# Kernel tuning notes

Measured on AMD Instinct MI355X. Metric: run time of the kernel, lower is better.

## Reference

```python
import jax, jax.numpy as jnp
import numpy as np

# Config constants (BayesianTripletConfig defaults)
MARGIN = 0.3
UNCERTAINTY_WEIGHT = 0.05
MIN_U = 1e-6
MAX_U = 1.0
TEMPERATURE = 1.0
EPS = 1e-8
B, D, N_CLASSES = 512, 256, 64


def setup_inputs() -> dict:
    key = jax.random.key(0)
    k1, k2, k3 = jax.random.split(key, 3)
    embeddings = jax.random.normal(k1, (B, D), dtype=jnp.float32)
    uncertainties = jax.random.uniform(k2, (B, D), dtype=jnp.float32)
    labels = jax.random.randint(k3, (B,), 0, N_CLASSES)
    return {"embeddings": embeddings, "uncertainties": uncertainties, "labels": labels}


def _loss(embeddings, uncertainties, labels):
    u = jnp.clip(uncertainties, MIN_U, MAX_U)
    u = jnp.where(jnp.isnan(u) | jnp.isinf(u), MIN_U, u)

    # ---- uncertainty-aware euclidean distances (vectorized) ----
    diff = embeddings[:, None, :] - embeddings[None, :, :]        # [B,B,D]
    dist = jnp.sqrt(jnp.sum(diff * diff, axis=-1)) + EPS           # [B,B]
    # d(dist_ij)/d(e_i,d) = diff_ijd / dist_ij ; propagate anchor-side uncertainty u_i
    partial = diff / dist[:, :, None]                              # [B,B,D]
    dist_unc = jnp.sqrt(jnp.sum(partial * partial * (u[:, None, :] ** 2), axis=-1) + EPS)  # [B,B]

    # ---- hardest triplet mining (vectorized over anchors) ----
    same = labels[:, None] == labels[None, :]
    eye = jnp.eye(labels.shape[0], dtype=bool)
    pos_mask = same & ~eye
    neg_mask = ~same
    neg_inf = jnp.float32(-1e30)
    pos_inf = jnp.float32(1e30)
    hardest_pos = jnp.argmax(jnp.where(pos_mask, dist, neg_inf), axis=1)  # farthest positive
    hardest_neg = jnp.argmin(jnp.where(neg_mask, dist, pos_inf), axis=1)  # closest negative
    valid = pos_mask.any(axis=1) & neg_mask.any(axis=1)

    rows = jnp.arange(labels.shape[0])
    d_pos = dist[rows, hardest_pos]
    d_neg = dist[rows, hardest_neg]
    u_pos = dist_unc[rows, hardest_pos]
    u_neg = dist_unc[rows, hardest_neg]

    # ---- probabilistic (gaussian) uncertainty-aware margin loss per triplet ----
    sigma = jnp.sqrt(u_pos ** 2 + u_neg ** 2 + EPS)
    margin_eff = MARGIN + UNCERTAINTY_WEIGHT * sigma               # adaptive_margin=True
    z = (d_pos - d_neg + margin_eff) / (sigma * TEMPERATURE)
    per_triplet = sigma * TEMPERATURE * jax.nn.softplus(z)         # smooth uncertainty-weighted hinge

    n_valid = jnp.maximum(jnp.sum(valid.astype(jnp.float32)), 1.0)
    main_loss = jnp.sum(jnp.where(valid, per_triplet, 0.0)) / n_valid

    # ---- uncertainty regularization (uncertainty_regularization=True) ----
    unc_reg = jnp.mean(u)
    total = main_loss + UNCERTAINTY_WEIGHT * unc_reg
    total = jnp.where(jnp.isnan(total) | jnp.isinf(total), 0.0, total)
    return total


def reference(embeddings, uncertainties, labels):
    return _loss(embeddings, uncertainties, labels)
```

## Files before the change

kernel.cpp:

```cpp
#include <hip/hip_runtime.h>
#include <math.h>

#define B 512
#define D 256
#define MARGIN 0.3f
#define UW 0.05f
#define MIN_U 1e-6f
#define EPS 1e-8f

#define TI 16
#define TJ 64
#define BK 64
#define NJT (B / TJ)

typedef unsigned long long ull;


static __device__ inline ull shfl_xor_u64(ull v, int m) {
    unsigned int lo = (unsigned int)v;
    unsigned int hi = (unsigned int)(v >> 32);
    lo = __shfl_xor(lo, m, 64);
    hi = __shfl_xor(hi, m, 64);
    return ((ull)hi << 32) | lo;
}

static __device__ inline ull bcast_u64_lane0(ull v) {
    unsigned int lo = (unsigned int)v;
    unsigned int hi = (unsigned int)(v >> 32);
    lo = (unsigned int)__shfl((int)lo, 0, 64);
    hi = (unsigned int)__shfl((int)hi, 0, 64);
    return ((ull)hi << 32) | lo;
}

__global__ __launch_bounds__(256) void dist_mine(const float* __restrict__ emb,
                                                 const int* __restrict__ labels,
                                                 ull* __restrict__ pmax_part,
                                                 ull* __restrict__ nmin_part,
                                                 unsigned int* __restrict__ counter) {
    const int jt = blockIdx.x;
    const int it = blockIdx.y;
    const int t  = threadIdx.x;
    const int row  = t >> 4;
    const int col4 = (t & 15) * 4;

    if (jt == 0 && it == 0 && t == 0) *counter = 0u;

    __shared__ float As[BK][TI + 1];
    __shared__ float Bs[BK][TJ + 4];
    __shared__ int labI[TI], labJ[TJ];

    const int gi0 = it * TI;
    const int gj0 = jt * TJ;
    if (t < TI) labI[t] = labels[gi0 + t];
    if (t < TJ) labJ[t] = labels[gj0 + t];

    float a0 = 0.f, a1 = 0.f, a2 = 0.f, a3 = 0.f;

    for (int kc = 0; kc < D; kc += BK) {
        __syncthreads();
        {
            const int r = t >> 4;
            const int f = t & 15;
            float4 v = *reinterpret_cast<const float4*>(&emb[(size_t)(gi0 + r) * D + kc + f * 4]);
            As[f * 4 + 0][r] = v.x;
            As[f * 4 + 1][r] = v.y;
            As[f * 4 + 2][r] = v.z;
            As[f * 4 + 3][r] = v.w;
        }
#pragma unroll
        for (int g = 0; g < 4; ++g) {
            const int r = g * 16 + (t >> 4);
            const int f = t & 15;
            float4 v = *reinterpret_cast<const float4*>(&emb[(size_t)(gj0 + r) * D + kc + f * 4]);
            Bs[f * 4 + 0][r] = v.x;
            Bs[f * 4 + 1][r] = v.y;
            Bs[f * 4 + 2][r] = v.z;
            Bs[f * 4 + 3][r] = v.w;
        }
        __syncthreads();
#pragma unroll 8
        for (int k = 0; k < BK; ++k) {
            float a = As[k][row];
            float4 b = *reinterpret_cast<const float4*>(&Bs[k][col4]);
            float d;
            d = a - b.x; a0 = fmaf(d, d, a0);
            d = a - b.y; a1 = fmaf(d, d, a1);
            d = a - b.z; a2 = fmaf(d, d, a2);
            d = a - b.w; a3 = fmaf(d, d, a3);
        }
    }

    const int gi = gi0 + row;
    const int li = labI[row];
    ull pbest = 0ull;
    ull nbest = ~0ull;
    float accs[4] = {a0, a1, a2, a3};
#pragma unroll
    for (int c = 0; c < 4; ++c) {
        const int jj = col4 + c;
        const int gj = gj0 + jj;
        const float dist = sqrtf(accs[c]) + EPS;
        const int lj = labJ[jj];
        const ull fb = (ull)__float_as_uint(dist) << 32;
        if (li == lj && gi != gj) {
            ull e = fb | (unsigned int)(0xFFFFFFFFu - (unsigned int)gj);
            pbest = pbest > e ? pbest : e;
        }
        if (li != lj) {
            ull e = fb | (unsigned int)gj;
            nbest = nbest < e ? nbest : e;
        }
    }
#pragma unroll
    for (int m = 1; m < 16; m <<= 1) {
        ull p2 = shfl_xor_u64(pbest, m);
        ull n2 = shfl_xor_u64(nbest, m);
        pbest = pbest > p2 ? pbest : p2;
        nbest = nbest < n2 ? nbest : n2;
    }
    if ((t & 15) == 0) {
        pmax_part[(size_t)jt * B + gi] = pbest;
        nmin_part[(size_t)jt * B + gi] = nbest;
    }
}

__global__ __launch_bounds__(256) void finalize(const float* __restrict__ emb,
                                                const float* __restrict__ unc,
                                                const ull* __restrict__ pmax_part,
                                                const ull* __restrict__ nmin_part,
                                                float* __restrict__ blk_part,
                                                unsigned int* __restrict__ counter,
                                                float* __restrict__ out) {
    const int t = threadIdx.x;
    const int wave = t >> 6;
    const int lane = t & 63;
    __shared__ float red[4][3];
    __shared__ int s_last;

    float loss_sum = 0.f, nval = 0.f, usum = 0.f;
    const float4* emb4 = reinterpret_cast<const float4*>(emb);
    const float4* unc4 = reinterpret_cast<const float4*>(unc);

#pragma unroll
    for (int a = 0; a < 2; ++a) {
        const int i = blockIdx.x * 8 + wave * 2 + a;

        ull pe = 0ull, ne = ~0ull;
        if (lane < NJT) {
            pe = pmax_part[(size_t)lane * B + i];
            ne = nmin_part[(size_t)lane * B + i];
        }
#pragma unroll
        for (int m = 1; m < NJT; m <<= 1) {
            ull p2 = shfl_xor_u64(pe, m);
            ull n2 = shfl_xor_u64(ne, m);
            pe = pe > p2 ? pe : p2;
            ne = ne < n2 ? ne : n2;
        }
        pe = bcast_u64_lane0(pe);
        ne = bcast_u64_lane0(ne);

        const bool valid = (pe != 0ull) && (ne != ~0ull);
        const int jp = valid ? (int)(0xFFFFFFFFu - (unsigned int)pe) : i;
        const int jn = valid ? (int)(unsigned int)ne : i;
        const float dp = __uint_as_float((unsigned int)(pe >> 32));
        const float dn = __uint_as_float((unsigned int)(ne >> 32));

        float4 e = emb4[(size_t)i * 64 + lane];
        float4 u = unc4[(size_t)i * 64 + lane];
        float4 p = emb4[(size_t)jp * 64 + lane];
        float4 n = emb4[(size_t)jn * 64 + lane];
        float ux = fminf(fmaxf(u.x, MIN_U), 1.0f);
        float uy = fminf(fmaxf(u.y, MIN_U), 1.0f);
        float uz = fminf(fmaxf(u.z, MIN_U), 1.0f);
        float uw_ = fminf(fmaxf(u.w, MIN_U), 1.0f);

        float s0, s1, s2, d;
        d = e.x - p.x; s0 = ux * ux * d * d;
        d = e.y - p.y; s0 = fmaf(uy * uy, d * d, s0);
        d = e.z - p.z; s0 = fmaf(uz * uz, d * d, s0);
        d = e.w - p.w; s0 = fmaf(uw_ * uw_, d * d, s0);
        d = e.x - n.x; s1 = ux * ux * d * d;
        d = e.y - n.y; s1 = fmaf(uy * uy, d * d, s1);
        d = e.z - n.z; s1 = fmaf(uz * uz, d * d, s1);
        d = e.w - n.w; s1 = fmaf(uw_ * uw_, d * d, s1);
        s2 = ux + uy + uz + uw_;

#pragma unroll
        for (int m = 1; m < 64; m <<= 1) {
            s0 += __shfl_xor(s0, m, 64);
            s1 += __shfl_xor(s1, m, 64);
            s2 += __shfl_xor(s2, m, 64);
        }

        if (lane == 0) {
            usum += s2;
            if (valid) {
                const float up2 = s0 / (dp * dp) + EPS;
                const float un2 = s1 / (dn * dn) + EPS;
                const float sigma = sqrtf(up2 + un2 + EPS);
                const float z = (dp - dn + MARGIN + UW * sigma) / sigma;
                const float sp = fmaxf(z, 0.f) + log1pf(expf(-fabsf(z)));
                loss_sum += sigma * sp;
                nval += 1.0f;
            }
        }
    }

    if (lane == 0) {
        red[wave][0] = loss_sum;
        red[wave][1] = nval;
        red[wave][2] = usum;
    }
    __syncthreads();
    if (t == 0) {
        float l = red[0][0] + red[1][0] + red[2][0] + red[3][0];
        float v = red[0][1] + red[1][1] + red[2][1] + red[3][1];
        float s = red[0][2] + red[1][2] + red[2][2] + red[3][2];
        __hip_atomic_store(&blk_part[blockIdx.x * 3 + 0], l, __ATOMIC_RELAXED, __HIP_MEMORY_SCOPE_AGENT);
        __hip_atomic_store(&blk_part[blockIdx.x * 3 + 1], v, __ATOMIC_RELAXED, __HIP_MEMORY_SCOPE_AGENT);
        __hip_atomic_store(&blk_part[blockIdx.x * 3 + 2], s, __ATOMIC_RELAXED, __HIP_MEMORY_SCOPE_AGENT);
        unsigned int done = __hip_atomic_fetch_add(counter, 1u, __ATOMIC_ACQ_REL, __HIP_MEMORY_SCOPE_AGENT);
        s_last = (done == 63u);
    }
    __syncthreads();

    if (s_last && wave == 0) {
        float l = __hip_atomic_load(&blk_part[lane * 3 + 0], __ATOMIC_RELAXED, __HIP_MEMORY_SCOPE_AGENT);
        float v = __hip_atomic_load(&blk_part[lane * 3 + 1], __ATOMIC_RELAXED, __HIP_MEMORY_SCOPE_AGENT);
        float s = __hip_atomic_load(&blk_part[lane * 3 + 2], __ATOMIC_RELAXED, __HIP_MEMORY_SCOPE_AGENT);
#pragma unroll
        for (int m = 1; m < 64; m <<= 1) {
            l += __shfl_xor(l, m, 64);
            v += __shfl_xor(v, m, 64);
            s += __shfl_xor(s, m, 64);
        }
        if (lane == 0) {
            float total = l / fmaxf(v, 1.0f) + UW * (s / (float)(B * D));
            if (!isfinite(total)) total = 0.f;
            out[0] = total;
        }
    }
}

extern "C" void kernel_launch(void* const* d_in, const int* in_sizes, int n_in,
                              void* d_out, int out_size, void* d_ws, size_t ws_size,
                              hipStream_t stream) {
    const float* emb = (const float*)d_in[0];
    const float* unc = (const float*)d_in[1];
    const int* labels = (const int*)d_in[2];
    float* out = (float*)d_out;

    char* ws = (char*)d_ws;
    ull* pmax_part = (ull*)(ws);
    ull* nmin_part = (ull*)(ws + 32768);
    float* blk_part = (float*)(ws + 65536);
    unsigned int* counter = (unsigned int*)(ws + 66304);

    dim3 grid(NJT, B / TI);
    dist_mine<<<grid, 256, 0, stream>>>(emb, labels, pmax_part, nmin_part, counter);
    finalize<<<64, 256, 0, stream>>>(emb, unc, pmax_part, nmin_part, blk_part, counter, out);
}
```

Measured before the change: 72.60 us.

## Fuse distance mining and finalize into one cooperative kernel with grid syncs

Merges the two kernels into a single cooperative launch of 256 blocks. A grid-wide sync separates the mining phase from the per-anchor loss phase, and a second grid sync replaces the last-block atomic counter for the final reduction. The aim is to remove the second kernel launch and its inter-kernel gap. In exchange it pays for two grid barriers, and only half the waves do work in the finalize phase. Block 0 now reduces 256 partials across four waves.

```diff
diff --git a/kernel.cpp b/kernel.cpp
--- a/kernel.cpp
+++ b/kernel.cpp
@@ -1,4 +1,5 @@
 #include <hip/hip_runtime.h>
+#include <hip/hip_cooperative_groups.h>
 #include <math.h>
 
 #define B 512
@@ -14,6 +15,7 @@
 #define NJT (B / TJ)
 
 typedef unsigned long long ull;
+namespace cg = cooperative_groups;
 
 
 static __device__ inline ull shfl_xor_u64(ull v, int m) {
@@ -32,22 +34,25 @@
     return ((ull)hi << 32) | lo;
 }
 
-__global__ __launch_bounds__(256) void dist_mine(const float* __restrict__ emb,
-                                                 const int* __restrict__ labels,
-                                                 ull* __restrict__ pmax_part,
-                                                 ull* __restrict__ nmin_part,
-                                                 unsigned int* __restrict__ counter) {
-    const int jt = blockIdx.x;
-    const int it = blockIdx.y;
+__global__ __launch_bounds__(256) void fused(const float* __restrict__ emb,
+                                             const float* __restrict__ unc,
+                                             const int* __restrict__ labels,
+                                             ull* __restrict__ pmax_part,
+                                             ull* __restrict__ nmin_part,
+                                             float* __restrict__ blk_part,
+                                             float* __restrict__ out) {
+    const int bid = blockIdx.x;
+    const int jt = bid & (NJT - 1);
+    const int it = bid >> 3;
     const int t  = threadIdx.x;
     const int row  = t >> 4;
     const int col4 = (t & 15) * 4;
 
-    if (jt == 0 && it == 0 && t == 0) *counter = 0u;
-
     __shared__ float As[BK][TI + 1];
     __shared__ float Bs[BK][TJ + 4];
     __shared__ int labI[TI], labJ[TJ];
+    __shared__ float red[2][3];
+    __shared__ float fred[4][3];
 
     const int gi0 = it * TI;
     const int gj0 = jt * TJ;
@@ -90,65 +95,54 @@
         }
     }
 
-    const int gi = gi0 + row;
-    const int li = labI[row];
-    ull pbest = 0ull;
-    ull nbest = ~0ull;
-    float accs[4] = {a0, a1, a2, a3};
-#pragma unroll
-    for (int c = 0; c < 4; ++c) {
-        const int jj = col4 + c;
-        const int gj = gj0 + jj;
-        const float dist = sqrtf(accs[c]) + EPS;
-        const int lj = labJ[jj];
-        const ull fb = (ull)__float_as_uint(dist) << 32;
-        if (li == lj && gi != gj) {
-            ull e = fb | (unsigned int)(0xFFFFFFFFu - (unsigned int)gj);
-            pbest = pbest > e ? pbest : e;
-        }
-        if (li != lj) {
-            ull e = fb | (unsigned int)gj;
-            nbest = nbest < e ? nbest : e;
-        }
-    }
-#pragma unroll
-    for (int m = 1; m < 16; m <<= 1) {
-        ull p2 = shfl_xor_u64(pbest, m);
-        ull n2 = shfl_xor_u64(nbest, m);
-        pbest = pbest > p2 ? pbest : p2;
-        nbest = nbest < n2 ? nbest : n2;
-    }
-    if ((t & 15) == 0) {
-        pmax_part[(size_t)jt * B + gi] = pbest;
-        nmin_part[(size_t)jt * B + gi] = nbest;
-    }
-}
-
-__global__ __launch_bounds__(256) void finalize(const float* __restrict__ emb,
-                                                const float* __restrict__ unc,
-                                                const ull* __restrict__ pmax_part,
-                                                const ull* __restrict__ nmin_part,
-                                                float* __restrict__ blk_part,
-                                                unsigned int* __restrict__ counter,
-                                                float* __restrict__ out) {
-    const int t = threadIdx.x;
+    {
+        const int gi = gi0 + row;
+        const int li = labI[row];
+        ull pbest = 0ull;
+        ull nbest = ~0ull;
+        float accs[4] = {a0, a1, a2, a3};
+#pragma unroll
+        for (int c = 0; c < 4; ++c) {
+            const int jj = col4 + c;
+            const int gj = gj0 + jj;
+            const float dist = sqrtf(accs[c]) + EPS;
+            const int lj = labJ[jj];
+            const ull fb = (ull)__float_as_uint(dist) << 32;
+            if (li == lj && gi != gj) {
+                ull e = fb | (unsigned int)(0xFFFFFFFFu - (unsigned int)gj);
+                pbest = pbest > e ? pbest : e;
+            }
+            if (li != lj) {
+                ull e = fb | (unsigned int)gj;
+                nbest = nbest < e ? nbest : e;
+            }
+        }
+#pragma unroll
+        for (int m = 1; m < 16; m <<= 1) {
+            ull p2 = shfl_xor_u64(pbest, m);
+            ull n2 = shfl_xor_u64(nbest, m);
+            pbest = pbest > p2 ? pbest : p2;
+            nbest = nbest < n2 ? nbest : n2;
+        }
+        if ((t & 15) == 0) {
+            __hip_atomic_store(&pmax_part[(size_t)jt * B + gi], pbest, __ATOMIC_RELAXED, __HIP_MEMORY_SCOPE_AGENT);
+            __hip_atomic_store(&nmin_part[(size_t)jt * B + gi], nbest, __ATOMIC_RELAXED, __HIP_MEMORY_SCOPE_AGENT);
+        }
+    }
+
+    cg::this_grid().sync();
+
     const int wave = t >> 6;
     const int lane = t & 63;
-    __shared__ float red[4][3];
-    __shared__ int s_last;
-
-    float loss_sum = 0.f, nval = 0.f, usum = 0.f;
-    const float4* emb4 = reinterpret_cast<const float4*>(emb);
-    const float4* unc4 = reinterpret_cast<const float4*>(unc);
-
-#pragma unroll
-    for (int a = 0; a < 2; ++a) {
-        const int i = blockIdx.x * 8 + wave * 2 + a;
+
+    if (wave < 2) {
+        const int i = bid * 2 + wave;
+        float loss_sum = 0.f, nval = 0.f, usum = 0.f;
 
         ull pe = 0ull, ne = ~0ull;
         if (lane < NJT) {
-            pe = pmax_part[(size_t)lane * B + i];
-            ne = nmin_part[(size_t)lane * B + i];
+            pe = __hip_atomic_load(&pmax_part[(size_t)lane * B + i], __ATOMIC_RELAXED, __HIP_MEMORY_SCOPE_AGENT);
+            ne = __hip_atomic_load(&nmin_part[(size_t)lane * B + i], __ATOMIC_RELAXED, __HIP_MEMORY_SCOPE_AGENT);
         }
 #pragma unroll
         for (int m = 1; m < NJT; m <<= 1) {
@@ -166,6 +160,8 @@
         const float dp = __uint_as_float((unsigned int)(pe >> 32));
         const float dn = __uint_as_float((unsigned int)(ne >> 32));
 
+        const float4* emb4 = reinterpret_cast<const float4*>(emb);
+        const float4* unc4 = reinterpret_cast<const float4*>(unc);
         float4 e = emb4[(size_t)i * 64 + lane];
         float4 u = unc4[(size_t)i * 64 + lane];
         float4 p = emb4[(size_t)jp * 64 + lane];
@@ -194,41 +190,34 @@
         }
 
         if (lane == 0) {
-            usum += s2;
+            usum = s2;
             if (valid) {
                 const float up2 = s0 / (dp * dp) + EPS;
                 const float un2 = s1 / (dn * dn) + EPS;
                 const float sigma = sqrtf(up2 + un2 + EPS);
                 const float z = (dp - dn + MARGIN + UW * sigma) / sigma;
                 const float sp = fmaxf(z, 0.f) + log1pf(expf(-fabsf(z)));
-                loss_sum += sigma * sp;
-                nval += 1.0f;
+                loss_sum = sigma * sp;
+                nval = 1.0f;
             }
-        }
-    }
-
-    if (lane == 0) {
-        red[wave][0] = loss_sum;
-        red[wave][1] = nval;
-        red[wave][2] = usum;
+            red[wave][0] = loss_sum;
+            red[wave][1] = nval;
+            red[wave][2] = usum;
+        }
     }
     __syncthreads();
     if (t == 0) {
-        float l = red[0][0] + red[1][0] + red[2][0] + red[3][0];
-        float v = red[0][1] + red[1][1] + red[2][1] + red[3][1];
-        float s = red[0][2] + red[1][2] + red[2][2] + red[3][2];
-        __hip_atomic_store(&blk_part[blockIdx.x * 3 + 0], l, __ATOMIC_RELAXED, __HIP_MEMORY_SCOPE_AGENT);
-        __hip_atomic_store(&blk_part[blockIdx.x * 3 + 1], v, __ATOMIC_RELAXED, __HIP_MEMORY_SCOPE_AGENT);
-        __hip_atomic_store(&blk_part[blockIdx.x * 3 + 2], s, __ATOMIC_RELAXED, __HIP_MEMORY_SCOPE_AGENT);
-        unsigned int done = __hip_atomic_fetch_add(counter, 1u, __ATOMIC_ACQ_REL, __HIP_MEMORY_SCOPE_AGENT);
-        s_last = (done == 63u);
-    }
-    __syncthreads();
-
-    if (s_last && wave == 0) {
-        float l = __hip_atomic_load(&blk_part[lane * 3 + 0], __ATOMIC_RELAXED, __HIP_MEMORY_SCOPE_AGENT);
-        float v = __hip_atomic_load(&blk_part[lane * 3 + 1], __ATOMIC_RELAXED, __HIP_MEMORY_SCOPE_AGENT);
-        float s = __hip_atomic_load(&blk_part[lane * 3 + 2], __ATOMIC_RELAXED, __HIP_MEMORY_SCOPE_AGENT);
+        __hip_atomic_store(&blk_part[bid * 3 + 0], red[0][0] + red[1][0], __ATOMIC_RELAXED, __HIP_MEMORY_SCOPE_AGENT);
+        __hip_atomic_store(&blk_part[bid * 3 + 1], red[0][1] + red[1][1], __ATOMIC_RELAXED, __HIP_MEMORY_SCOPE_AGENT);
+        __hip_atomic_store(&blk_part[bid * 3 + 2], red[0][2] + red[1][2], __ATOMIC_RELAXED, __HIP_MEMORY_SCOPE_AGENT);
+    }
+
+    cg::this_grid().sync();
+
+    if (bid == 0) {
+        float l = __hip_atomic_load(&blk_part[t * 3 + 0], __ATOMIC_RELAXED, __HIP_MEMORY_SCOPE_AGENT);
+        float v = __hip_atomic_load(&blk_part[t * 3 + 1], __ATOMIC_RELAXED, __HIP_MEMORY_SCOPE_AGENT);
+        float s = __hip_atomic_load(&blk_part[t * 3 + 2], __ATOMIC_RELAXED, __HIP_MEMORY_SCOPE_AGENT);
 #pragma unroll
         for (int m = 1; m < 64; m <<= 1) {
             l += __shfl_xor(l, m, 64);
@@ -236,6 +225,15 @@
             s += __shfl_xor(s, m, 64);
         }
         if (lane == 0) {
+            fred[wave][0] = l;
+            fred[wave][1] = v;
+            fred[wave][2] = s;
+        }
+        __syncthreads();
+        if (t == 0) {
+            l = fred[0][0] + fred[1][0] + fred[2][0] + fred[3][0];
+            v = fred[0][1] + fred[1][1] + fred[2][1] + fred[3][1];
+            s = fred[0][2] + fred[1][2] + fred[2][2] + fred[3][2];
             float total = l / fmaxf(v, 1.0f) + UW * (s / (float)(B * D));
             if (!isfinite(total)) total = 0.f;
             out[0] = total;
@@ -255,9 +253,8 @@
     ull* pmax_part = (ull*)(ws);
     ull* nmin_part = (ull*)(ws + 32768);
     float* blk_part = (float*)(ws + 65536);
-    unsigned int* counter = (unsigned int*)(ws + 66304);
-
-    dim3 grid(NJT, B / TI);
-    dist_mine<<<grid, 256, 0, stream>>>(emb, labels, pmax_part, nmin_part, counter);
-    finalize<<<64, 256, 0, stream>>>(emb, unc, pmax_part, nmin_part, blk_part, counter, out);
-}
+
+    void* args[] = {(void*)&emb, (void*)&unc, (void*)&labels,
+                    (void*)&pmax_part, (void*)&nmin_part, (void*)&blk_part, (void*)&out};
+    hipLaunchCooperativeKernel((void*)fused, dim3(256), dim3(256), args, 0, stream);
+}
```

Result: slower. 131.0 us (+80.5%).
